# Kernel tuning notes

Measured on AMD Instinct MI355X. Metric: run time of the kernel, lower is better.

Reference implementation:

```python
import jax, jax.numpy as jnp
import numpy as np

VOCAB = 100000; D = 300; F_NUM = 768
M = 64; N = 16
SURF_L = 4; CTX_L = 50; DOC_L = 100; BODY_L = 200
HEADS = 5


def _conv_relu_avg(x, W, b):
    # x: [B, L, D] tokens-embedded; conv1d (valid) + relu + global avgpool -> [B, F]
    y = jax.lax.conv_general_dilated(x.transpose(0, 2, 1), W, (1,), 'VALID',
                                     dimension_numbers=('NCH', 'OIH', 'NCH'))
    return jax.nn.relu(y + b[None, :, None]).mean(axis=2)


def _mha(q, k, v, num_heads=HEADS):
    # split-head scaled dot-product attention (no learned projections), q:[Lq,D] k,v:[Lk,D]
    Lq, Dm = q.shape
    hd = Dm // num_heads
    qh = q.reshape(Lq, num_heads, hd).transpose(1, 0, 2)
    kh = k.reshape(k.shape[0], num_heads, hd).transpose(1, 0, 2)
    vh = v.reshape(v.shape[0], num_heads, hd).transpose(1, 0, 2)
    att = jax.nn.softmax(jnp.einsum('hqd,hkd->hqk', qh, kh) * (1.0 / np.sqrt(hd)), axis=-1)
    out = jnp.einsum('hqk,hkd->hqd', att, vh)
    return out.transpose(1, 0, 2).reshape(Lq, Dm)


def _cos(a, b, eps=1e-6):
    na = jnp.maximum(jnp.sqrt((a * a).sum(-1)), eps)
    nb = jnp.maximum(jnp.sqrt((b * b).sum(-1)), eps)
    return (a * b).sum(-1) / (na * nb)


def setup_inputs() -> dict:
    key = jax.random.key(0)
    ks = jax.random.split(key, 20)
    inp = {}
    inp['mention_entity'] = jnp.ones((M, N), dtype=jnp.int32)
    inp['m'] = M
    inp['n'] = N
    inp['mention_vec'] = jax.random.randint(ks[0], (M, SURF_L), 0, VOCAB)
    inp['context_vec'] = jax.random.randint(ks[1], (M, CTX_L), 0, VOCAB)
    inp['doc_vec'] = jax.random.randint(ks[2], (DOC_L,), 0, VOCAB)
    inp['title_vec'] = jax.random.normal(ks[3], (N, F_NUM), dtype=jnp.float32)
    inp['body_vec'] = jax.random.randint(ks[4], (N, BODY_L), 0, VOCAB)
    inp['sfeats'] = jnp.zeros((N, 1), dtype=jnp.float32)
    inp['m2c_prior'] = jax.random.uniform(ks[5], (N,), dtype=jnp.float32)
    inp['men2cands'] = jax.random.randint(ks[6], (M, N), 0, VOCAB)
    inp['contexts_ids'] = jax.random.randint(ks[7], (M, CTX_L), 0, VOCAB)
    inp['hand_features'] = jax.random.uniform(ks[8], (N, 1), dtype=jnp.float32)
    inp['bert_doc_vec'] = jax.random.normal(ks[9], (1, F_NUM), dtype=jnp.float32)
    # learned parameters
    inp['embed_table'] = jax.random.normal(ks[10], (VOCAB, D), dtype=jnp.float32) * 0.1
    inp['conv_ms_w'] = jax.random.normal(ks[11], (F_NUM, D, 2), dtype=jnp.float32) * 0.05
    inp['conv_ms_b'] = jnp.zeros((F_NUM,), dtype=jnp.float32)
    inp['conv_mc_w'] = jax.random.normal(ks[12], (F_NUM, D, 5), dtype=jnp.float32) * 0.05
    inp['conv_mc_b'] = jnp.zeros((F_NUM,), dtype=jnp.float32)
    inp['layer_local_w'] = jax.random.normal(ks[13], (7,), dtype=jnp.float32) * 0.3
    inp['layer_local_b'] = jnp.zeros((), dtype=jnp.float32)
    inp['att_w1'] = jax.random.normal(ks[14], (600, 300), dtype=jnp.float32) * 0.05
    inp['att_b1'] = jnp.zeros((300,), dtype=jnp.float32)
    inp['att_w2'] = jax.random.normal(ks[15], (300, 1), dtype=jnp.float32) * 0.05
    inp['att_b2'] = jnp.zeros((), dtype=jnp.float32)
    return inp


def reference(mention_entity, m, n, mention_vec, context_vec, doc_vec, title_vec,
              body_vec, sfeats, m2c_prior, men2cands, contexts_ids, hand_features,
              bert_doc_vec, embed_table, conv_ms_w, conv_ms_b, conv_mc_w, conv_mc_b,
              layer_local_w, layer_local_b, att_w1, att_b1, att_w2, att_b2):
    # per-mention conv features (vectorized over all mentions at once)
    ms = _conv_relu_avg(embed_table[mention_vec], conv_ms_w, conv_ms_b)   # [M,768]
    mc = _conv_relu_avg(embed_table[context_vec], conv_mc_w, conv_mc_b)   # [M,768]
    md = bert_doc_vec[0]                                                  # [768]
    doc_emb = embed_table[doc_vec]                                        # [100,300]
    body_emb = embed_table[body_vec]                                      # [N,200,300]

    # per-candidate cross attention doc<->body, max-pooled over query positions
    att_d_b = jax.vmap(lambda b: _mha(doc_emb, b, b).max(axis=0))(body_emb)          # [N,300]
    att_b_d = jax.vmap(lambda b: _mha(b, doc_emb, doc_emb).max(axis=0))(body_emb)    # [N,300]
    comb = jnp.concatenate([att_d_b, att_b_d], axis=-1)                              # [N,600]
    att_score = jax.nn.sigmoid(jax.nn.relu(comb @ att_w1 + att_b1) @ att_w2 + att_b2)[:, 0]  # [N]

    # LocalCtxAttRanker: candidate-vs-context attention score
    ctx_emb = embed_table[contexts_ids]                                   # [M,50,300]
    cand_emb = embed_table[men2cands]                                     # [M,N,300]
    tok = jnp.einsum('mnd,mtd->mnt', cand_emb, ctx_emb)                   # [M,N,50]
    p = jax.nn.softmax(tok.max(axis=1), axis=-1)                          # [M,50]
    ctxv = jnp.einsum('mt,mtd->md', p, ctx_emb)                           # [M,300]
    local_att = jnp.einsum('mnd,md->mn', cand_emb, ctxv)                  # [M,N]

    cos_st = _cos(ms[:, None, :], title_vec[None, :, :])                  # [M,N]
    cos_dt = _cos(md[None, :], title_vec)                                 # [N]
    cos_ct = _cos(mc[:, None, :], title_vec[None, :, :])                  # [M,N]

    Mm = ms.shape[0]
    bc = lambda v: jnp.broadcast_to(v[None, :], (Mm, v.shape[0]))
    # feature order matches torch.cat((hand_fea, prior, localAtt, attScore, C_score))
    feats = jnp.stack([bc(hand_features[:, 0]), bc(m2c_prior), local_att,
                       bc(att_score), cos_st, bc(cos_dt), cos_ct], axis=-1)  # [M,N,7]
    score = feats @ layer_local_w + layer_local_b                         # [M,N]

    # per-mention standardization (unbiased std, as torch.std), softmax and uniform renorm
    mu = score.mean(axis=1, keepdims=True)
    sd = score.std(axis=1, keepdims=True, ddof=1)
    z = (score - mu) / sd
    sm = jax.nn.softmax(z, axis=1)
    zmin = z.min(axis=1, keepdims=True)
    zmax = z.max(axis=1, keepdims=True)
    u = (z + 1.0 - zmin) / (zmax - zmin)
    u = u / u.sum(axis=1, keepdims=True)
    return (z, sm, u)
```

## Files before the change

### kernel.cpp

```cpp
#include <hip/hip_runtime.h>

#define MM 64
#define NN 16
#define DDIM 300
#define FNUM 768
#define SURF_LL 4
#define CTX_LL 50
#define DOC_LL 100
#define BODY_LL 200
#define NHEADS 5
#define HDIM 60

#define GM 2944
#define GK 1536
#define GN 768

typedef unsigned short u16;
typedef unsigned int u32;
typedef __attribute__((ext_vector_type(8))) short short8;
typedef __attribute__((ext_vector_type(4))) float f32x4;

#define OFF_MSG    0
#define OFF_CTX2G  76800
#define OFF_CANDG  1036800
#define OFF_MS     1344000
#define OFF_MC     1393152
#define OFF_PV0    1442304
#define OFF_PV1    1461504
#define OFF_ASC    1495104
#define OFF_LATT   1495120
#define OFF_ABF    1496144
#define OFF_WTMC   (OFF_ABF + GM*GK/2)
#define OFF_WTMS   (OFF_WTMC + GN*GK/2)

__device__ __forceinline__ u16 f2bf(float x) {
  union { float f; u32 u; } v; v.f = x;
  u32 r = v.u + 0x7FFFu + ((v.u >> 16) & 1u);
  return (u16)(r >> 16);
}

#define PREP_GATHER_END  1313
#define PREP_MCZ_END     1361
#define PREP_LOGIT       1361
#define PREP_ABUILD_BEG  1362
#define PREP_ABUILD_END  3570
#define PREP_WTMC_END    4338
#define PREP_WTMS_END    4458

__global__ __launch_bounds__(256) void mega_prep_kernel(
    const float* __restrict__ embed,
    const int* __restrict__ mention_vec,
    const int* __restrict__ context_vec,
    const int* __restrict__ contexts_ids,
    const int* __restrict__ men2cands,
    const float* __restrict__ Wmc,
    const float* __restrict__ Wms,
    float* __restrict__ dst, float* __restrict__ mc,
    float* __restrict__ att_logit,
    u32* __restrict__ Abf, u32* __restrict__ WTmc, float* __restrict__ WTms) {
  __shared__ float psm[4160];
  int bid = blockIdx.x;
  int tid = threadIdx.x;
  if (bid < PREP_GATHER_END) {
    int e4 = bid * 256 + tid;
    if (e4 < 4480 * 75) {
      int row = e4 / 75, c4 = e4 - row * 75;
      int tok;
      if (row < 256)       tok = mention_vec[row];
      else if (row < 3456) tok = contexts_ids[row - 256];
      else                 tok = men2cands[row - 3456];
      float4 v = *(const float4*)(embed + (size_t)tok * DDIM + c4 * 4);
      *(float4*)(dst + (size_t)row * DDIM + c4 * 4) = v;
    }
  } else if (bid < PREP_MCZ_END) {
    int e4 = (bid - PREP_GATHER_END) * 256 + tid;
    *(float4*)(mc + e4 * 4) = make_float4(0.f, 0.f, 0.f, 0.f);
  } else if (bid == PREP_LOGIT) {
    if (tid < NN) att_logit[tid] = 0.f;
  } else if (bid < PREP_ABUILD_END) {
    int idx4 = (bid - PREP_ABUILD_BEG) * 256 + tid;
    int r = idx4 / (GK / 8);
    int kq = idx4 - r * (GK / 8);
    int m = r / 46, t = r - m * 46;
    int kbase = kq * 8;
    u32 wlo[4];
#pragma unroll
    for (int q = 0; q < 4; q++) {
      u32 outw = 0;
#pragma unroll
      for (int j = 0; j < 2; j++) {
        int kj = kbase + q * 2 + j;
        u16 h = 0;
        if (kj < 1500) {
          int tap = kj / 300;
          int d = kj - tap * 300;
          int tok = context_vec[m * CTX_LL + t + tap];
          h = f2bf(embed[(size_t)tok * DDIM + d]);
        }
        outw |= (u32)h << (16 * j);
      }
      wlo[q] = outw;
    }
    ((uint4*)Abf)[idx4] = make_uint4(wlo[0], wlo[1], wlo[2], wlo[3]);
  } else if (bid < PREP_WTMC_END) {
    int n = bid - PREP_ABUILD_END;
    for (int i = tid; i < 1500; i += 256) psm[i] = Wmc[(size_t)n * 1500 + i];
    __syncthreads();
    for (int kp = tid; kp < GK / 2; kp += 256) {
      u32 outw = 0;
#pragma unroll
      for (int j = 0; j < 2; j++) {
        int kj = kp * 2 + j;
        u16 h = 0;
        if (kj < 1500) {
          int tap = kj / 300;
          int d = kj - tap * 300;
          h = f2bf(psm[d * 5 + tap]);
        }
        outw |= (u32)h << (16 * j);
      }
      WTmc[(size_t)n * (GK / 2) + kp] = outw;
    }
  } else {
    int tile = bid - PREP_WTMC_END;
    int kt = tile / 12, ft = tile - kt * 12;
    int k0 = kt * 64, f0 = ft * 64;
    for (int idx = tid; idx < 64 * 64; idx += 256) {
      int i = idx >> 6, j = idx & 63;
      if (k0 + j < 600)
        psm[j * 65 + i] = Wms[(size_t)(f0 + i) * 600 + (k0 + j)];
    }
    __syncthreads();
    for (int idx = tid; idx < 64 * 64; idx += 256) {
      int j = idx >> 6, i = idx & 63;
      if (k0 + j < 600)
        WTms[(size_t)(k0 + j) * FNUM + (f0 + i)] = psm[j * 65 + i];
    }
  }
}

__device__ __forceinline__ void conv_gemm_body(
    const u16* __restrict__ A,
    const u16* __restrict__ B,
    const float* __restrict__ bias,
    float* __restrict__ mc, int g, float* __restrict__ smem) {
  int bn = g % (GN / 64), bm = g / (GN / 64);
  u16* As = (u16*)smem;
  u16* Bs = (u16*)(smem + 2304);
  int tid = threadIdx.x;
  int w = tid >> 6, lane = tid & 63;
  int wr = w >> 1, wc = w & 1;
  int lg = lane >> 4, lm = lane & 15;
  f32x4 acc[2][2];
#pragma unroll
  for (int i = 0; i < 2; i++)
#pragma unroll
    for (int j = 0; j < 2; j++) acc[i][j] = (f32x4)0.f;
  int c0row = tid >> 3, ck = (tid & 7) * 8;
  const u16* Ag = A + (size_t)(bm * 64) * GK;
  const u16* Bg = B + (size_t)(bn * 64) * GK;
  for (int kt = 0; kt < GK / 64; kt++) {
    int k0 = kt * 64;
    uint4 av0 = *(const uint4*)(Ag + (size_t)c0row * GK + k0 + ck);
    uint4 av1 = *(const uint4*)(Ag + (size_t)(c0row + 32) * GK + k0 + ck);
    uint4 bv0 = *(const uint4*)(Bg + (size_t)c0row * GK + k0 + ck);
    uint4 bv1 = *(const uint4*)(Bg + (size_t)(c0row + 32) * GK + k0 + ck);
    __syncthreads();
    *(uint4*)&As[c0row * 72 + ck] = av0;
    *(uint4*)&As[(c0row + 32) * 72 + ck] = av1;
    *(uint4*)&Bs[c0row * 72 + ck] = bv0;
    *(uint4*)&Bs[(c0row + 32) * 72 + ck] = bv1;
    __syncthreads();
#pragma unroll
    for (int kk = 0; kk < 2; kk++) {
      short8 af0 = *(const short8*)&As[(wr * 32 + lm) * 72 + kk * 32 + lg * 8];
      short8 af1 = *(const short8*)&As[(wr * 32 + 16 + lm) * 72 + kk * 32 + lg * 8];
      short8 bf0 = *(const short8*)&Bs[(wc * 32 + lm) * 72 + kk * 32 + lg * 8];
      short8 bf1 = *(const short8*)&Bs[(wc * 32 + 16 + lm) * 72 + kk * 32 + lg * 8];
      acc[0][0] = __builtin_amdgcn_mfma_f32_16x16x32_bf16(af0, bf0, acc[0][0], 0, 0, 0);
      acc[0][1] = __builtin_amdgcn_mfma_f32_16x16x32_bf16(af0, bf1, acc[0][1], 0, 0, 0);
      acc[1][0] = __builtin_amdgcn_mfma_f32_16x16x32_bf16(af1, bf0, acc[1][0], 0, 0, 0);
      acc[1][1] = __builtin_amdgcn_mfma_f32_16x16x32_bf16(af1, bf1, acc[1][1], 0, 0, 0);
    }
  }
#pragma unroll
  for (int mf = 0; mf < 2; mf++)
#pragma unroll
    for (int nf = 0; nf < 2; nf++) {
      int col = bn * 64 + wc * 32 + nf * 16 + lm;
      float bb = bias[col];
      int base = bm * 64 + wr * 32 + mf * 16 + lg * 4;
      int mcur = base / 46;
      float s = 0.f;
#pragma unroll
      for (int r = 0; r < 4; r++) {
        float v = fmaxf(acc[mf][nf][r] + bb, 0.f) * (1.0f / 46.0f);
        int mm = (base + r) / 46;
        if (mm != mcur) { atomicAdd(&mc[mcur * FNUM + col], s); s = 0.f; mcur = mm; }
        s += v;
      }
      atomicAdd(&mc[mcur * FNUM + col], s);
    }
}

__device__ __forceinline__ void conv_ms_body(
    const float* __restrict__ msg, const float* __restrict__ WT,
    const float* __restrict__ B, float* __restrict__ ms, int b) {
  int m = b / 3, fi = b - m * 3;
  int f = fi * 256 + threadIdx.x;
  const float* x = msg + m * SURF_LL * DDIM;
  float a0 = 0.f, a1 = 0.f, a2 = 0.f;
  for (int d = 0; d < DDIM; d++) {
    float v0 = x[d], v1 = x[DDIM + d], v2 = x[2 * DDIM + d], v3 = x[3 * DDIM + d];
    float wA = WT[(size_t)(2 * d) * FNUM + f];
    float wB = WT[(size_t)(2 * d + 1) * FNUM + f];
    a0 += v0 * wA + v1 * wB;
    a1 += v1 * wA + v2 * wB;
    a2 += v2 * wA + v3 * wB;
  }
  float bb = B[f];
  float r = fmaxf(a0 + bb, 0.f) + fmaxf(a1 + bb, 0.f) + fmaxf(a2 + bb, 0.f);
  ms[m * FNUM + f] = r * (1.0f / 3.0f);
}

template <int DIR>
__device__ __forceinline__ void scores_pv_body(
    const float* __restrict__ embed, const int* __restrict__ doc_vec,
    const int* __restrict__ body_vec, float* __restrict__ pvp, int b,
    float* __restrict__ smem) {
  constexpr int Lq = DIR ? 200 : 100;
  constexpr int Lk = DIR ? 100 : 200;
  constexpr int KPL = DIR ? 2 : 4;
  constexpr int NQT = DIR ? 7 : 4;
  constexpr int NHALF = DIR ? 1 : 2;
  int qt = b / 80;
  int rem = b - qt * 80;
  int n = rem / 5, h = rem - n * 5;
  const int* qids = DIR ? body_vec + n * BODY_LL : doc_vec;
  const int* kids = DIR ? doc_vec : body_vec + n * BODY_LL;
  float* Ks = smem;
  float* Qs = smem + 12400;
  float* Pl = smem + 12400;
  float* red = smem + 15600;
  for (int idx = threadIdx.x; idx < Lk * 15; idx += 256) {
    int r = idx / 15, c = idx - r * 15;
    float4 v = *(const float4*)(embed + (size_t)kids[r] * DDIM + h * HDIM + c * 4);
    float* dp = Ks + r * 62 + c * 4;
    dp[0] = v.x; dp[1] = v.y; dp[2] = v.z; dp[3] = v.w;
  }
  for (int idx = threadIdx.x; idx < 32 * 15; idx += 256) {
    int r = idx / 15, c = idx - r * 15;
    int q = qt * 32 + r; if (q >= Lq) q = Lq - 1;
    float4 v = *(const float4*)(embed + (size_t)qids[q] * DDIM + h * HDIM + c * 4);
    float* dp = Qs + r * 64 + c * 4;
    dp[0] = v.x; dp[1] = v.y; dp[2] = v.z; dp[3] = v.w;
  }
  __syncthreads();
  int w = threadIdx.x >> 6, lane = threadIdx.x & 63;
  int kcl[KPL];
#pragma unroll
  for (int j = 0; j < KPL; j++) {
    int kk = lane + 64 * j; kcl[j] = (kk < Lk) ? kk : (Lk - 1);
  }
  float acc[8][KPL];
#pragma unroll
  for (int i = 0; i < 8; i++)
#pragma unroll
    for (int j = 0; j < KPL; j++) acc[i][j] = 0.f;
  for (int d = 0; d < HDIM; d += 4) {
    float2 kva[KPL], kvb[KPL];
#pragma unroll
    for (int j = 0; j < KPL; j++) {
      kva[j] = *(const float2*)&Ks[kcl[j] * 62 + d];
      kvb[j] = *(const float2*)&Ks[kcl[j] * 62 + d + 2];
    }
#pragma unroll
    for (int i = 0; i < 8; i++) {
      float4 qv = *(const float4*)&Qs[(w * 8 + i) * 64 + d];
#pragma unroll
      for (int j = 0; j < KPL; j++)
        acc[i][j] += qv.x * kva[j].x + qv.y * kva[j].y +
                     qv.z * kvb[j].x + qv.w * kvb[j].y;
    }
  }
  const float scale = 0.12909944487358056f;
#pragma unroll
  for (int i = 0; i < 8; i++) {
    float mx = -1e30f;
#pragma unroll
    for (int j = 0; j < KPL; j++)
      if (lane + 64 * j < Lk) mx = fmaxf(mx, acc[i][j]);
#pragma unroll
    for (int o = 32; o >= 1; o >>= 1) mx = fmaxf(mx, __shfl_xor(mx, o));
    float mxs = mx * scale;
    float p[KPL];
    float s = 0.f;
#pragma unroll
    for (int j = 0; j < KPL; j++) {
      p[j] = (lane + 64 * j < Lk) ? __expf(acc[i][j] * scale - mxs) : 0.f;
      s += p[j];
    }
#pragma unroll
    for (int o = 32; o >= 1; o >>= 1) s += __shfl_xor(s, o);
    float inv = 1.0f / s;
#pragma unroll
    for (int j = 0; j < KPL; j++) acc[i][j] = p[j] * inv;
  }
  __syncthreads();
  float o[8];
#pragma unroll
  for (int i = 0; i < 8; i++) o[i] = 0.f;
  int dl = (lane < HDIM) ? lane : (HDIM - 1);
#pragma unroll
  for (int half = 0; half < NHALF; half++) {
    int kbase = half * 100;
#pragma unroll
    for (int j = 0; j < KPL; j++) {
      int kk = lane + 64 * j;
      int rel = kk - kbase;
      if (rel >= 0 && rel < 100 && kk < Lk) {
#pragma unroll
        for (int i = 0; i < 8; i++)
          Pl[(w * 8 + i) * 100 + rel] = acc[i][j];
      }
    }
    for (int k4 = 0; k4 < 25; k4++) {
      int k = kbase + k4 * 4;
      float kv0 = Ks[(k + 0) * 62 + dl];
      float kv1 = Ks[(k + 1) * 62 + dl];
      float kv2 = Ks[(k + 2) * 62 + dl];
      float kv3 = Ks[(k + 3) * 62 + dl];
#pragma unroll
      for (int i = 0; i < 8; i++) {
        float4 pq = *(const float4*)&Pl[(w * 8 + i) * 100 + k4 * 4];
        o[i] += pq.x * kv0 + pq.y * kv1 + pq.z * kv2 + pq.w * kv3;
      }
    }
  }
  float omax = -1e30f;
#pragma unroll
  for (int i = 0; i < 8; i++) {
    int q = qt * 32 + w * 8 + i;
    if (q < Lq) omax = fmaxf(omax, o[i]);
  }
  red[w * 64 + lane] = omax;
  __syncthreads();
  if (threadIdx.x < 64 && lane < HDIM) {
    float m4 = fmaxf(fmaxf(red[0 * 64 + lane], red[1 * 64 + lane]),
                     fmaxf(red[2 * 64 + lane], red[3 * 64 + lane]));
    pvp[((size_t)(n * NHEADS + h) * NQT + qt) * HDIM + lane] = m4;
  }
}

__device__ __forceinline__ void tokctxv_body(
    const float* __restrict__ candg, const float* __restrict__ ctx2g,
    float* __restrict__ local_att, int m, float* __restrict__ smem) {
  float* cand  = smem;
  float* ctx   = smem + 4800;
  float* tokb  = smem + 9600;
  float* tkmx  = smem + 9872;
  float* pp    = smem + 9936;
  float* sctxv = smem + 10000;
  int tid = threadIdx.x;
  for (int i = tid; i < NN * DDIM; i += 256)
    cand[i] = candg[(size_t)m * NN * DDIM + i];
  int nI = tid >> 4, tt = tid & 15;
  for (int tile = 0; tile < 4; tile++) {
    int cbase = tile * 16;
    __syncthreads();
    for (int i = tid; i < 16 * DDIM; i += 256) {
      int rr = i / DDIM, cc = i - rr * DDIM;
      int t = cbase + rr;
      ctx[rr * DDIM + cc] = (t < CTX_LL) ? ctx2g[(size_t)(m * CTX_LL + t) * DDIM + cc] : 0.f;
    }
    __syncthreads();
    const float4* ca = (const float4*)(cand + nI * DDIM);
    const float4* cb = (const float4*)(ctx + tt * DDIM);
    float dsum = 0.f;
#pragma unroll
    for (int c = 0; c < 75; c++) {
      float4 a = ca[c], b = cb[c];
      dsum += a.x * b.x + a.y * b.y + a.z * b.z + a.w * b.w;
    }
    tokb[nI * 17 + tt] = dsum;
    __syncthreads();
    if (tid < 16) {
      float mx = -1e30f;
      for (int nn = 0; nn < NN; nn++) mx = fmaxf(mx, tokb[nn * 17 + tid]);
      int t = cbase + tid;
      if (t < CTX_LL) tkmx[t] = mx;
    }
  }
  __syncthreads();
  if (tid < 64) {
    float v = (tid < CTX_LL) ? tkmx[tid] : -1e30f;
    float mx = v;
#pragma unroll
    for (int o = 32; o >= 1; o >>= 1) mx = fmaxf(mx, __shfl_xor(mx, o));
    float e = (tid < CTX_LL) ? expf(v - mx) : 0.f;
    float s = e;
#pragma unroll
    for (int o = 32; o >= 1; o >>= 1) s += __shfl_xor(s, o);
    pp[tid] = e / s;
  }
  __syncthreads();
  for (int d = tid; d < DDIM; d += 256) {
    float acc = 0.f;
    for (int t = 0; t < CTX_LL; t++)
      acc += pp[t] * ctx2g[(size_t)(m * CTX_LL + t) * DDIM + d];
    sctxv[d] = acc;
  }
  __syncthreads();
  int j = tid & 15;
  float dd = 0.f;
  for (int i = j; i < DDIM; i += 16) dd += cand[nI * DDIM + i] * sctxv[i];
#pragma unroll
  for (int o = 8; o >= 1; o >>= 1) dd += __shfl_xor(dd, o);
  if (j == 0) local_att[m * NN + nI] = dd;
}

__global__ __launch_bounds__(256) void mega_mid_kernel(
    const float* __restrict__ embed,
    const int* __restrict__ doc_vec,
    const int* __restrict__ body_vec,
    const float* __restrict__ msg,
    const float* __restrict__ WTms,
    const float* __restrict__ Bms,
    const float* __restrict__ candg,
    const float* __restrict__ ctx2g,
    const u16* __restrict__ Abf,
    const u16* __restrict__ WTmc,
    const float* __restrict__ Bmc,
    float* __restrict__ ms,
    float* __restrict__ mc,
    float* __restrict__ pv0,
    float* __restrict__ pv1,
    float* __restrict__ local_att) {
  __shared__ float smem[15856];
  int bid = blockIdx.x;
  if (bid < 192) {
    conv_ms_body(msg, WTms, Bms, ms, bid);
  } else if (bid < 512) {
    scores_pv_body<0>(embed, doc_vec, body_vec, pv0, bid - 192, smem);
  } else if (bid < 1072) {
    scores_pv_body<1>(embed, doc_vec, body_vec, pv1, bid - 512, smem);
  } else if (bid < 1136) {
    tokctxv_body(candg, ctx2g, local_att, bid - 1072, smem);
  } else {
    conv_gemm_body(Abf, WTmc, Bmc, mc, bid - 1136, smem);
  }
}

__global__ __launch_bounds__(256) void mlp_kernel(
    const float* __restrict__ pv0, const float* __restrict__ pv1,
    const float* __restrict__ w1, const float* __restrict__ b1,
    const float* __restrict__ w2,
    float* __restrict__ att_logit) {
  int bid = blockIdx.x;
  int n = bid / 5, jc = bid - n * 5;
  int tid = threadIdx.x;
  __shared__ float comb[600];
  __shared__ float partial[4][64];
  for (int idx = tid; idx < 600; idx += 256) {
    int side = idx >= 300;
    int pos = idx - side * 300;
    int h = pos / 60, d = pos - h * 60;
    float mx = -1e30f;
    if (!side) {
#pragma unroll
      for (int pt = 0; pt < 4; pt++)
        mx = fmaxf(mx, pv0[(size_t)((n * NHEADS + h) * 4 + pt) * HDIM + d]);
    } else {
#pragma unroll
      for (int pt = 0; pt < 7; pt++)
        mx = fmaxf(mx, pv1[(size_t)((n * NHEADS + h) * 7 + pt) * HDIM + d]);
    }
    comb[idx] = mx;
  }
  __syncthreads();
  int w = tid >> 6, lane = tid & 63;
  int jl = (lane < 60) ? lane : 59;
  int jg = jc * 60 + jl;
  float acc = 0.f;
  for (int k = w; k < 600; k += 4)
    acc += comb[k] * w1[(size_t)k * 300 + jg];
  partial[w][lane] = acc;
  __syncthreads();
  if (tid < 64) {
    float hv = partial[0][lane] + partial[1][lane] +
               partial[2][lane] + partial[3][lane];
    float hj = fmaxf(hv + b1[jg], 0.f) * w2[jg];
    if (lane >= 60) hj = 0.f;
#pragma unroll
    for (int o = 32; o >= 1; o >>= 1) hj += __shfl_xor(hj, o);
    if (lane == 0) atomicAdd(&att_logit[n], hj);
  }
}

__global__ __launch_bounds__(256) void final_kernel(
    const float* __restrict__ ms,
    const float* __restrict__ mc,
    const float* __restrict__ title,
    const float* __restrict__ bert,
    const float* __restrict__ att_logit,
    const float* __restrict__ b2,
    const float* __restrict__ m2c_prior,
    const float* __restrict__ hand,
    const float* __restrict__ local_att,
    const float* __restrict__ w7,
    const float* __restrict__ b7,
    float* __restrict__ out) {
  int m = blockIdx.x, tid = threadIdx.x;
  __shared__ float sms[FNUM], smc[FNUM], smd[FNUM];
  __shared__ float snorm[3], sscore[16], wred[3][4];
  for (int i = tid; i < FNUM; i += 256) {
    sms[i] = ms[m * FNUM + i];
    smc[i] = mc[m * FNUM + i];
    smd[i] = bert[i];
  }
  __syncthreads();
  float p1 = 0.f, p2 = 0.f, p3 = 0.f;
  for (int i = tid; i < FNUM; i += 256) {
    float a = sms[i], b = smc[i], c = smd[i];
    p1 += a * a; p2 += b * b; p3 += c * c;
  }
#pragma unroll
  for (int o = 32; o >= 1; o >>= 1) {
    p1 += __shfl_xor(p1, o); p2 += __shfl_xor(p2, o); p3 += __shfl_xor(p3, o);
  }
  int wid = tid >> 6, lane = tid & 63;
  if (lane == 0) { wred[0][wid] = p1; wred[1][wid] = p2; wred[2][wid] = p3; }
  __syncthreads();
  if (tid == 0) {
    snorm[0] = fmaxf(sqrtf(wred[0][0] + wred[0][1] + wred[0][2] + wred[0][3]), 1e-6f);
    snorm[1] = fmaxf(sqrtf(wred[1][0] + wred[1][1] + wred[1][2] + wred[1][3]), 1e-6f);
    snorm[2] = fmaxf(sqrtf(wred[2][0] + wred[2][1] + wred[2][2] + wred[2][3]), 1e-6f);
  }
  __syncthreads();
  int nI = tid >> 4, j = tid & 15;
  float d1 = 0.f, d2 = 0.f, d3 = 0.f, d4 = 0.f;
  for (int i = j; i < FNUM; i += 16) {
    float t = title[nI * FNUM + i];
    d1 += sms[i] * t; d2 += smc[i] * t; d3 += smd[i] * t; d4 += t * t;
  }
#pragma unroll
  for (int o = 8; o >= 1; o >>= 1) {
    d1 += __shfl_xor(d1, o); d2 += __shfl_xor(d2, o);
    d3 += __shfl_xor(d3, o); d4 += __shfl_xor(d4, o);
  }
  if (j == 0) {
    float nt = fmaxf(sqrtf(d4), 1e-6f);
    float cos_st = d1 / (snorm[0] * nt);
    float cos_ct = d2 / (snorm[1] * nt);
    float cos_dt = d3 / (snorm[2] * nt);
    float asc = 1.0f / (1.0f + expf(-(att_logit[nI] + b2[0])));
    float score = hand[nI] * w7[0] + m2c_prior[nI] * w7[1] +
                  local_att[m * NN + nI] * w7[2] + asc * w7[3] +
                  cos_st * w7[4] + cos_dt * w7[5] + cos_ct * w7[6] + b7[0];
    sscore[nI] = score;
  }
  __syncthreads();
  if (tid < 16) {
    float x = sscore[tid];
    float s = x;
#pragma unroll
    for (int o = 8; o >= 1; o >>= 1) s += __shfl_xor(s, o);
    float mu = s * (1.0f / 16.0f);
    float dv = (x - mu) * (x - mu);
    float vs = dv;
#pragma unroll
    for (int o = 8; o >= 1; o >>= 1) vs += __shfl_xor(vs, o);
    float sd = sqrtf(vs * (1.0f / 15.0f));
    float z = (x - mu) / sd;
    float zm = z;
#pragma unroll
    for (int o = 8; o >= 1; o >>= 1) zm = fmaxf(zm, __shfl_xor(zm, o));
    float e = expf(z - zm);
    float es = e;
#pragma unroll
    for (int o = 8; o >= 1; o >>= 1) es += __shfl_xor(es, o);
    float sm = e / es;
    float zmin = z;
#pragma unroll
    for (int o = 8; o >= 1; o >>= 1) zmin = fminf(zmin, __shfl_xor(zmin, o));
    float u0 = (z + 1.0f - zmin) / (zm - zmin);
    float us = u0;
#pragma unroll
    for (int o = 8; o >= 1; o >>= 1) us += __shfl_xor(us, o);
    float u = u0 / us;
    out[m * NN + tid] = z;
    out[MM * NN + m * NN + tid] = sm;
    out[2 * MM * NN + m * NN + tid] = u;
  }
}

extern "C" void kernel_launch(void* const* d_in, const int* in_sizes, int n_in,
                              void* d_out, int out_size, void* d_ws, size_t ws_size,
                              hipStream_t stream) {
  const int*   mention_vec   = (const int*)d_in[3];
  const int*   context_vec   = (const int*)d_in[4];
  const int*   doc_vec       = (const int*)d_in[5];
  const float* title_vec     = (const float*)d_in[6];
  const int*   body_vec      = (const int*)d_in[7];
  const float* m2c_prior     = (const float*)d_in[9];
  const int*   men2cands     = (const int*)d_in[10];
  const int*   contexts_ids  = (const int*)d_in[11];
  const float* hand_features = (const float*)d_in[12];
  const float* bert_doc_vec  = (const float*)d_in[13];
  const float* embed_table   = (const float*)d_in[14];
  const float* conv_ms_w     = (const float*)d_in[15];
  const float* conv_ms_b     = (const float*)d_in[16];
  const float* conv_mc_w     = (const float*)d_in[17];
  const float* conv_mc_b     = (const float*)d_in[18];
  const float* layer_local_w = (const float*)d_in[19];
  const float* layer_local_b = (const float*)d_in[20];
  const float* att_w1        = (const float*)d_in[21];
  const float* att_b1        = (const float*)d_in[22];
  const float* att_w2        = (const float*)d_in[23];
  const float* att_b2        = (const float*)d_in[24];

  float* ws     = (float*)d_ws;
  float* msg    = ws + OFF_MSG;
  float* ctx2g  = ws + OFF_CTX2G;
  float* candg  = ws + OFF_CANDG;
  float* ms     = ws + OFF_MS;
  float* mc     = ws + OFF_MC;
  float* pv0    = ws + OFF_PV0;
  float* pv1    = ws + OFF_PV1;
  float* att_lg = ws + OFF_ASC;
  float* latt   = ws + OFF_LATT;
  u16*   Abf    = (u16*)(ws + OFF_ABF);
  u16*   WTmc   = (u16*)(ws + OFF_WTMC);
  float* WTms   = ws + OFF_WTMS;
  float* out    = (float*)d_out;

  mega_prep_kernel<<<dim3(PREP_WTMS_END), dim3(256), 0, stream>>>(
      embed_table, mention_vec, context_vec, contexts_ids, men2cands,
      conv_mc_w, conv_ms_w, ws, mc, att_lg, (u32*)Abf, (u32*)WTmc, WTms);
  mega_mid_kernel<<<dim3(1688), dim3(256), 0, stream>>>(
      embed_table, doc_vec, body_vec, msg, WTms, conv_ms_b, candg, ctx2g,
      Abf, WTmc, conv_mc_b, ms, mc, pv0, pv1, latt);
  mlp_kernel<<<dim3(80), dim3(256), 0, stream>>>(
      pv0, pv1, att_w1, att_b1, att_w2, att_lg);
  final_kernel<<<dim3(MM), dim3(256), 0, stream>>>(
      ms, mc, title_vec, bert_doc_vec, att_lg, att_b2, m2c_prior,
      hand_features, latt, layer_local_w, layer_local_b, out);
}
```

Measured before the change: 376.3 us.

## Launch mid kernel with 512 threads and split attention rows across eight waves

Doubles the mid mega-kernel block size to 512 threads. The attention score/PV body now spreads its 32 query rows over eight waves of four rows each instead of four waves of eight, and reduces the per-wave maxima across eight waves. The GEMM body uses the extra threads only for tile loads, and the conv_ms and tokctxv bodies mostly mask off or duplicate work in the upper half. This is meant to cut per-wave serial work and register pressure in the attention path, at the cost of idle or redundant waves in the other bodies and a tighter register budget under the 512-thread launch bound.

Result: slower. 439.4 us (+16.7%).

```diff
diff --git a/kernel.cpp b/kernel.cpp
--- a/kernel.cpp
+++ b/kernel.cpp
@@ -149,7 +149,7 @@
   u16* Bs = (u16*)(smem + 2304);
   int tid = threadIdx.x;
   int w = tid >> 6, lane = tid & 63;
-  int wr = w >> 1, wc = w & 1;
+  int wr = (w >> 1) & 1, wc = w & 1;
   int lg = lane >> 4, lm = lane & 15;
   f32x4 acc[2][2];
 #pragma unroll
@@ -161,53 +161,53 @@
   const u16* Bg = B + (size_t)(bn * 64) * GK;
   for (int kt = 0; kt < GK / 64; kt++) {
     int k0 = kt * 64;
-    uint4 av0 = *(const uint4*)(Ag + (size_t)c0row * GK + k0 + ck);
-    uint4 av1 = *(const uint4*)(Ag + (size_t)(c0row + 32) * GK + k0 + ck);
-    uint4 bv0 = *(const uint4*)(Bg + (size_t)c0row * GK + k0 + ck);
-    uint4 bv1 = *(const uint4*)(Bg + (size_t)(c0row + 32) * GK + k0 + ck);
+    uint4 av = *(const uint4*)(Ag + (size_t)c0row * GK + k0 + ck);
+    uint4 bv = *(const uint4*)(Bg + (size_t)c0row * GK + k0 + ck);
     __syncthreads();
-    *(uint4*)&As[c0row * 72 + ck] = av0;
-    *(uint4*)&As[(c0row + 32) * 72 + ck] = av1;
-    *(uint4*)&Bs[c0row * 72 + ck] = bv0;
-    *(uint4*)&Bs[(c0row + 32) * 72 + ck] = bv1;
+    *(uint4*)&As[c0row * 72 + ck] = av;
+    *(uint4*)&Bs[c0row * 72 + ck] = bv;
     __syncthreads();
-#pragma unroll
-    for (int kk = 0; kk < 2; kk++) {
-      short8 af0 = *(const short8*)&As[(wr * 32 + lm) * 72 + kk * 32 + lg * 8];
-      short8 af1 = *(const short8*)&As[(wr * 32 + 16 + lm) * 72 + kk * 32 + lg * 8];
-      short8 bf0 = *(const short8*)&Bs[(wc * 32 + lm) * 72 + kk * 32 + lg * 8];
-      short8 bf1 = *(const short8*)&Bs[(wc * 32 + 16 + lm) * 72 + kk * 32 + lg * 8];
-      acc[0][0] = __builtin_amdgcn_mfma_f32_16x16x32_bf16(af0, bf0, acc[0][0], 0, 0, 0);
-      acc[0][1] = __builtin_amdgcn_mfma_f32_16x16x32_bf16(af0, bf1, acc[0][1], 0, 0, 0);
-      acc[1][0] = __builtin_amdgcn_mfma_f32_16x16x32_bf16(af1, bf0, acc[1][0], 0, 0, 0);
-      acc[1][1] = __builtin_amdgcn_mfma_f32_16x16x32_bf16(af1, bf1, acc[1][1], 0, 0, 0);
-    }
-  }
-#pragma unroll
-  for (int mf = 0; mf < 2; mf++)
-#pragma unroll
-    for (int nf = 0; nf < 2; nf++) {
-      int col = bn * 64 + wc * 32 + nf * 16 + lm;
-      float bb = bias[col];
-      int base = bm * 64 + wr * 32 + mf * 16 + lg * 4;
-      int mcur = base / 46;
-      float s = 0.f;
-#pragma unroll
-      for (int r = 0; r < 4; r++) {
-        float v = fmaxf(acc[mf][nf][r] + bb, 0.f) * (1.0f / 46.0f);
-        int mm = (base + r) / 46;
-        if (mm != mcur) { atomicAdd(&mc[mcur * FNUM + col], s); s = 0.f; mcur = mm; }
-        s += v;
+    if (w < 4) {
+#pragma unroll
+      for (int kk = 0; kk < 2; kk++) {
+        short8 af0 = *(const short8*)&As[(wr * 32 + lm) * 72 + kk * 32 + lg * 8];
+        short8 af1 = *(const short8*)&As[(wr * 32 + 16 + lm) * 72 + kk * 32 + lg * 8];
+        short8 bf0 = *(const short8*)&Bs[(wc * 32 + lm) * 72 + kk * 32 + lg * 8];
+        short8 bf1 = *(const short8*)&Bs[(wc * 32 + 16 + lm) * 72 + kk * 32 + lg * 8];
+        acc[0][0] = __builtin_amdgcn_mfma_f32_16x16x32_bf16(af0, bf0, acc[0][0], 0, 0, 0);
+        acc[0][1] = __builtin_amdgcn_mfma_f32_16x16x32_bf16(af0, bf1, acc[0][1], 0, 0, 0);
+        acc[1][0] = __builtin_amdgcn_mfma_f32_16x16x32_bf16(af1, bf0, acc[1][0], 0, 0, 0);
+        acc[1][1] = __builtin_amdgcn_mfma_f32_16x16x32_bf16(af1, bf1, acc[1][1], 0, 0, 0);
       }
-      atomicAdd(&mc[mcur * FNUM + col], s);
-    }
+    }
+  }
+  if (w < 4) {
+#pragma unroll
+    for (int mf = 0; mf < 2; mf++)
+#pragma unroll
+      for (int nf = 0; nf < 2; nf++) {
+        int col = bn * 64 + wc * 32 + nf * 16 + lm;
+        float bb = bias[col];
+        int base = bm * 64 + wr * 32 + mf * 16 + lg * 4;
+        int mcur = base / 46;
+        float s = 0.f;
+#pragma unroll
+        for (int r = 0; r < 4; r++) {
+          float v = fmaxf(acc[mf][nf][r] + bb, 0.f) * (1.0f / 46.0f);
+          int mm = (base + r) / 46;
+          if (mm != mcur) { atomicAdd(&mc[mcur * FNUM + col], s); s = 0.f; mcur = mm; }
+          s += v;
+        }
+        atomicAdd(&mc[mcur * FNUM + col], s);
+      }
+  }
 }
 
 __device__ __forceinline__ void conv_ms_body(
     const float* __restrict__ msg, const float* __restrict__ WT,
     const float* __restrict__ B, float* __restrict__ ms, int b) {
   int m = b / 3, fi = b - m * 3;
-  int f = fi * 256 + threadIdx.x;
+  int f = fi * 256 + (threadIdx.x & 255);
   const float* x = msg + m * SURF_LL * DDIM;
   float a0 = 0.f, a1 = 0.f, a2 = 0.f;
   for (int d = 0; d < DDIM; d++) {
@@ -220,7 +220,7 @@
   }
   float bb = B[f];
   float r = fmaxf(a0 + bb, 0.f) + fmaxf(a1 + bb, 0.f) + fmaxf(a2 + bb, 0.f);
-  ms[m * FNUM + f] = r * (1.0f / 3.0f);
+  if (threadIdx.x < 256) ms[m * FNUM + f] = r * (1.0f / 3.0f);
 }
 
 template <int DIR>
@@ -242,13 +242,13 @@
   float* Qs = smem + 12400;
   float* Pl = smem + 12400;
   float* red = smem + 15600;
-  for (int idx = threadIdx.x; idx < Lk * 15; idx += 256) {
+  for (int idx = threadIdx.x; idx < Lk * 15; idx += 512) {
     int r = idx / 15, c = idx - r * 15;
     float4 v = *(const float4*)(embed + (size_t)kids[r] * DDIM + h * HDIM + c * 4);
     float* dp = Ks + r * 62 + c * 4;
     dp[0] = v.x; dp[1] = v.y; dp[2] = v.z; dp[3] = v.w;
   }
-  for (int idx = threadIdx.x; idx < 32 * 15; idx += 256) {
+  for (int idx = threadIdx.x; idx < 32 * 15; idx += 512) {
     int r = idx / 15, c = idx - r * 15;
     int q = qt * 32 + r; if (q >= Lq) q = Lq - 1;
     float4 v = *(const float4*)(embed + (size_t)qids[q] * DDIM + h * HDIM + c * 4);
@@ -262,9 +262,9 @@
   for (int j = 0; j < KPL; j++) {
     int kk = lane + 64 * j; kcl[j] = (kk < Lk) ? kk : (Lk - 1);
   }
-  float acc[8][KPL];
-#pragma unroll
-  for (int i = 0; i < 8; i++)
+  float acc[4][KPL];
+#pragma unroll
+  for (int i = 0; i < 4; i++)
 #pragma unroll
     for (int j = 0; j < KPL; j++) acc[i][j] = 0.f;
   for (int d = 0; d < HDIM; d += 4) {
@@ -275,8 +275,8 @@
       kvb[j] = *(const float2*)&Ks[kcl[j] * 62 + d + 2];
     }
 #pragma unroll
-    for (int i = 0; i < 8; i++) {
-      float4 qv = *(const float4*)&Qs[(w * 8 + i) * 64 + d];
+    for (int i = 0; i < 4; i++) {
+      float4 qv = *(const float4*)&Qs[(w * 4 + i) * 64 + d];
 #pragma unroll
       for (int j = 0; j < KPL; j++)
         acc[i][j] += qv.x * kva[j].x + qv.y * kva[j].y +
@@ -285,7 +285,7 @@
   }
   const float scale = 0.12909944487358056f;
 #pragma unroll
-  for (int i = 0; i < 8; i++) {
+  for (int i = 0; i < 4; i++) {
     float mx = -1e30f;
 #pragma unroll
     for (int j = 0; j < KPL; j++)
@@ -307,9 +307,9 @@
     for (int j = 0; j < KPL; j++) acc[i][j] = p[j] * inv;
   }
   __syncthreads();
-  float o[8];
-#pragma unroll
-  for (int i = 0; i < 8; i++) o[i] = 0.f;
+  float o[4];
+#pragma unroll
+  for (int i = 0; i < 4; i++) o[i] = 0.f;
   int dl = (lane < HDIM) ? lane : (HDIM - 1);
 #pragma unroll
   for (int half = 0; half < NHALF; half++) {
@@ -320,8 +320,8 @@
       int rel = kk - kbase;
       if (rel >= 0 && rel < 100 && kk < Lk) {
 #pragma unroll
-        for (int i = 0; i < 8; i++)
-          Pl[(w * 8 + i) * 100 + rel] = acc[i][j];
+        for (int i = 0; i < 4; i++)
+          Pl[(w * 4 + i) * 100 + rel] = acc[i][j];
       }
     }
     for (int k4 = 0; k4 < 25; k4++) {
@@ -331,23 +331,24 @@
       float kv2 = Ks[(k + 2) * 62 + dl];
       float kv3 = Ks[(k + 3) * 62 + dl];
 #pragma unroll
-      for (int i = 0; i < 8; i++) {
-        float4 pq = *(const float4*)&Pl[(w * 8 + i) * 100 + k4 * 4];
+      for (int i = 0; i < 4; i++) {
+        float4 pq = *(const float4*)&Pl[(w * 4 + i) * 100 + k4 * 4];
         o[i] += pq.x * kv0 + pq.y * kv1 + pq.z * kv2 + pq.w * kv3;
       }
     }
   }
   float omax = -1e30f;
 #pragma unroll
-  for (int i = 0; i < 8; i++) {
-    int q = qt * 32 + w * 8 + i;
+  for (int i = 0; i < 4; i++) {
+    int q = qt * 32 + w * 4 + i;
     if (q < Lq) omax = fmaxf(omax, o[i]);
   }
   red[w * 64 + lane] = omax;
   __syncthreads();
   if (threadIdx.x < 64 && lane < HDIM) {
-    float m4 = fmaxf(fmaxf(red[0 * 64 + lane], red[1 * 64 + lane]),
-                     fmaxf(red[2 * 64 + lane], red[3 * 64 + lane]));
+    float m4 = red[lane];
+#pragma unroll
+    for (int ww = 1; ww < 8; ww++) m4 = fmaxf(m4, red[ww * 64 + lane]);
     pvp[((size_t)(n * NHEADS + h) * NQT + qt) * HDIM + lane] = m4;
   }
 }
@@ -362,13 +363,14 @@
   float* pp    = smem + 9936;
   float* sctxv = smem + 10000;
   int tid = threadIdx.x;
-  for (int i = tid; i < NN * DDIM; i += 256)
+  int t2 = tid & 255;
+  for (int i = tid; i < NN * DDIM; i += 512)
     cand[i] = candg[(size_t)m * NN * DDIM + i];
-  int nI = tid >> 4, tt = tid & 15;
+  int nI = t2 >> 4, tt = t2 & 15;
   for (int tile = 0; tile < 4; tile++) {
     int cbase = tile * 16;
     __syncthreads();
-    for (int i = tid; i < 16 * DDIM; i += 256) {
+    for (int i = tid; i < 16 * DDIM; i += 512) {
       int rr = i / DDIM, cc = i - rr * DDIM;
       int t = cbase + rr;
       ctx[rr * DDIM + cc] = (t < CTX_LL) ? ctx2g[(size_t)(m * CTX_LL + t) * DDIM + cc] : 0.f;
@@ -404,22 +406,22 @@
     pp[tid] = e / s;
   }
   __syncthreads();
-  for (int d = tid; d < DDIM; d += 256) {
+  for (int d = tid; d < DDIM; d += 512) {
     float acc = 0.f;
     for (int t = 0; t < CTX_LL; t++)
       acc += pp[t] * ctx2g[(size_t)(m * CTX_LL + t) * DDIM + d];
     sctxv[d] = acc;
   }
   __syncthreads();
-  int j = tid & 15;
+  int j = t2 & 15;
   float dd = 0.f;
   for (int i = j; i < DDIM; i += 16) dd += cand[nI * DDIM + i] * sctxv[i];
 #pragma unroll
   for (int o = 8; o >= 1; o >>= 1) dd += __shfl_xor(dd, o);
-  if (j == 0) local_att[m * NN + nI] = dd;
-}
-
-__global__ __launch_bounds__(256) void mega_mid_kernel(
+  if (j == 0 && tid < 256) local_att[m * NN + nI] = dd;
+}
+
+__global__ __launch_bounds__(512) void mega_mid_kernel(
     const float* __restrict__ embed,
     const int* __restrict__ doc_vec,
     const int* __restrict__ body_vec,
@@ -436,7 +438,7 @@
     float* __restrict__ pv0,
     float* __restrict__ pv1,
     float* __restrict__ local_att) {
-  __shared__ float smem[15856];
+  __shared__ float smem[16112];
   int bid = blockIdx.x;
   if (bid < 192) {
     conv_ms_body(msg, WTms, Bms, ms, bid);
@@ -637,7 +639,7 @@
   mega_prep_kernel<<<dim3(PREP_WTMS_END), dim3(256), 0, stream>>>(
       embed_table, mention_vec, context_vec, contexts_ids, men2cands,
       conv_mc_w, conv_ms_w, ws, mc, att_lg, (u32*)Abf, (u32*)WTmc, WTms);
-  mega_mid_kernel<<<dim3(1688), dim3(256), 0, stream>>>(
+  mega_mid_kernel<<<dim3(1688), dim3(512), 0, stream>>>(
       embed_table, doc_vec, body_vec, msg, WTms, conv_ms_b, candg, ctx2g,
       Abf, WTmc, conv_mc_b, ms, mc, pv0, pv1, latt);
   mlp_kernel<<<dim3(80), dim3(256), 0, stream>>>(
```

## Split doc-query attention over key halves and shrink mid-kernel shared memory

Applied to the files above, without the earlier changes.

The doc-to-body attention (200 keys) is now split into two 100-key blocks, each storing unnormalized partial outputs plus softmax max and sum. The MLP kernel merges these flash-style before taking the per-position max. The candidate tile in the local-attention body is read straight from global memory instead of being staged in LDS. Together these cut the mid kernel's static shared memory from about 62KB to 38KB, raising occupancy and adding parallel blocks. The cost is extra partial-result traffic and a serial 100-step merge loop per element in the MLP kernel.

Measured after the change: 469.9 us. +24.9%, slower.

```diff
diff --git a/kernel.cpp b/kernel.cpp
--- a/kernel.cpp
+++ b/kernel.cpp
@@ -25,13 +25,14 @@
 #define OFF_CANDG  1036800
 #define OFF_MS     1344000
 #define OFF_MC     1393152
-#define OFF_PV0    1442304
 #define OFF_PV1    1461504
 #define OFF_ASC    1495104
 #define OFF_LATT   1495120
 #define OFF_ABF    1496144
 #define OFF_WTMC   (OFF_ABF + GM*GK/2)
 #define OFF_WTMS   (OFF_WTMC + GN*GK/2)
+#define OFF_PV0P   4807760
+#define PV0P_UNIT  1984
 
 __device__ __forceinline__ u16 f2bf(float x) {
   union { float f; u32 u; } v; v.f = x;
@@ -223,26 +224,19 @@
   ms[m * FNUM + f] = r * (1.0f / 3.0f);
 }
 
-template <int DIR>
-__device__ __forceinline__ void scores_pv_body(
+template <int MODE>
+__device__ __forceinline__ void attn_body(
     const float* __restrict__ embed, const int* __restrict__ doc_vec,
-    const int* __restrict__ body_vec, float* __restrict__ pvp, int b,
-    float* __restrict__ smem) {
-  constexpr int Lq = DIR ? 200 : 100;
-  constexpr int Lk = DIR ? 100 : 200;
-  constexpr int KPL = DIR ? 2 : 4;
-  constexpr int NQT = DIR ? 7 : 4;
-  constexpr int NHALF = DIR ? 1 : 2;
-  int qt = b / 80;
-  int rem = b - qt * 80;
-  int n = rem / 5, h = rem - n * 5;
-  const int* qids = DIR ? body_vec + n * BODY_LL : doc_vec;
-  const int* kids = DIR ? doc_vec : body_vec + n * BODY_LL;
+    const int* __restrict__ body_vec, float* __restrict__ outp,
+    int qt, int n, int h, int khalf, float* __restrict__ smem) {
+  constexpr int Lq = MODE ? 200 : 100;
+  const int* qids = MODE ? body_vec + n * BODY_LL : doc_vec;
+  const int* kids = MODE ? doc_vec : body_vec + n * BODY_LL + khalf * 100;
   float* Ks = smem;
-  float* Qs = smem + 12400;
-  float* Pl = smem + 12400;
-  float* red = smem + 15600;
-  for (int idx = threadIdx.x; idx < Lk * 15; idx += 256) {
+  float* Qs = smem + 6200;
+  float* Pl = smem + 6200;
+  float* red = smem + 9400;
+  for (int idx = threadIdx.x; idx < 100 * 15; idx += 256) {
     int r = idx / 15, c = idx - r * 15;
     float4 v = *(const float4*)(embed + (size_t)kids[r] * DDIM + h * HDIM + c * 4);
     float* dp = Ks + r * 62 + c * 4;
@@ -257,54 +251,42 @@
   }
   __syncthreads();
   int w = threadIdx.x >> 6, lane = threadIdx.x & 63;
-  int kcl[KPL];
-#pragma unroll
-  for (int j = 0; j < KPL; j++) {
-    int kk = lane + 64 * j; kcl[j] = (kk < Lk) ? kk : (Lk - 1);
-  }
-  float acc[8][KPL];
-#pragma unroll
-  for (int i = 0; i < 8; i++)
-#pragma unroll
-    for (int j = 0; j < KPL; j++) acc[i][j] = 0.f;
+  int kc0 = lane;
+  bool k1ok = (lane + 64 < 100);
+  int kc1 = k1ok ? lane + 64 : 99;
+  float acc[8][2];
+#pragma unroll
+  for (int i = 0; i < 8; i++) { acc[i][0] = 0.f; acc[i][1] = 0.f; }
   for (int d = 0; d < HDIM; d += 4) {
-    float2 kva[KPL], kvb[KPL];
-#pragma unroll
-    for (int j = 0; j < KPL; j++) {
-      kva[j] = *(const float2*)&Ks[kcl[j] * 62 + d];
-      kvb[j] = *(const float2*)&Ks[kcl[j] * 62 + d + 2];
-    }
+    float2 a0 = *(const float2*)&Ks[kc0 * 62 + d];
+    float2 b0 = *(const float2*)&Ks[kc0 * 62 + d + 2];
+    float2 a1 = *(const float2*)&Ks[kc1 * 62 + d];
+    float2 b1 = *(const float2*)&Ks[kc1 * 62 + d + 2];
 #pragma unroll
     for (int i = 0; i < 8; i++) {
       float4 qv = *(const float4*)&Qs[(w * 8 + i) * 64 + d];
-#pragma unroll
-      for (int j = 0; j < KPL; j++)
-        acc[i][j] += qv.x * kva[j].x + qv.y * kva[j].y +
-                     qv.z * kvb[j].x + qv.w * kvb[j].y;
+      acc[i][0] += qv.x * a0.x + qv.y * a0.y + qv.z * b0.x + qv.w * b0.y;
+      acc[i][1] += qv.x * a1.x + qv.y * a1.y + qv.z * b1.x + qv.w * b1.y;
     }
   }
   const float scale = 0.12909944487358056f;
+  float msv[8], ssv[8];
 #pragma unroll
   for (int i = 0; i < 8; i++) {
-    float mx = -1e30f;
-#pragma unroll
-    for (int j = 0; j < KPL; j++)
-      if (lane + 64 * j < Lk) mx = fmaxf(mx, acc[i][j]);
+    float mx = acc[i][0];
+    if (k1ok) mx = fmaxf(mx, acc[i][1]);
 #pragma unroll
     for (int o = 32; o >= 1; o >>= 1) mx = fmaxf(mx, __shfl_xor(mx, o));
     float mxs = mx * scale;
-    float p[KPL];
-    float s = 0.f;
-#pragma unroll
-    for (int j = 0; j < KPL; j++) {
-      p[j] = (lane + 64 * j < Lk) ? __expf(acc[i][j] * scale - mxs) : 0.f;
-      s += p[j];
-    }
+    float p0 = __expf(acc[i][0] * scale - mxs);
+    float p1 = k1ok ? __expf(acc[i][1] * scale - mxs) : 0.f;
+    float s = p0 + p1;
 #pragma unroll
     for (int o = 32; o >= 1; o >>= 1) s += __shfl_xor(s, o);
+    msv[i] = mxs; ssv[i] = s;
     float inv = 1.0f / s;
-#pragma unroll
-    for (int j = 0; j < KPL; j++) acc[i][j] = p[j] * inv;
+    acc[i][0] = p0 * inv;
+    acc[i][1] = p1 * inv;
   }
   __syncthreads();
   float o[8];
@@ -312,59 +294,64 @@
   for (int i = 0; i < 8; i++) o[i] = 0.f;
   int dl = (lane < HDIM) ? lane : (HDIM - 1);
 #pragma unroll
-  for (int half = 0; half < NHALF; half++) {
-    int kbase = half * 100;
-#pragma unroll
-    for (int j = 0; j < KPL; j++) {
-      int kk = lane + 64 * j;
-      int rel = kk - kbase;
-      if (rel >= 0 && rel < 100 && kk < Lk) {
-#pragma unroll
-        for (int i = 0; i < 8; i++)
-          Pl[(w * 8 + i) * 100 + rel] = acc[i][j];
+  for (int i = 0; i < 8; i++) Pl[(w * 8 + i) * 100 + lane] = acc[i][0];
+  if (k1ok) {
+#pragma unroll
+    for (int i = 0; i < 8; i++) Pl[(w * 8 + i) * 100 + lane + 64] = acc[i][1];
+  }
+  for (int k4 = 0; k4 < 25; k4++) {
+    int k = k4 * 4;
+    float kv0 = Ks[(k + 0) * 62 + dl];
+    float kv1 = Ks[(k + 1) * 62 + dl];
+    float kv2 = Ks[(k + 2) * 62 + dl];
+    float kv3 = Ks[(k + 3) * 62 + dl];
+#pragma unroll
+    for (int i = 0; i < 8; i++) {
+      float4 pq = *(const float4*)&Pl[(w * 8 + i) * 100 + k4 * 4];
+      o[i] += pq.x * kv0 + pq.y * kv1 + pq.z * kv2 + pq.w * kv3;
+    }
+  }
+  if constexpr (MODE == 0) {
+    if (lane < HDIM) {
+#pragma unroll
+      for (int i = 0; i < 8; i++)
+        outp[(w * 8 + i) * HDIM + lane] = o[i];
+    }
+    if (lane == 0) {
+#pragma unroll
+      for (int i = 0; i < 8; i++) {
+        outp[1920 + w * 8 + i] = msv[i];
+        outp[1952 + w * 8 + i] = ssv[i];
       }
     }
-    for (int k4 = 0; k4 < 25; k4++) {
-      int k = kbase + k4 * 4;
-      float kv0 = Ks[(k + 0) * 62 + dl];
-      float kv1 = Ks[(k + 1) * 62 + dl];
-      float kv2 = Ks[(k + 2) * 62 + dl];
-      float kv3 = Ks[(k + 3) * 62 + dl];
-#pragma unroll
-      for (int i = 0; i < 8; i++) {
-        float4 pq = *(const float4*)&Pl[(w * 8 + i) * 100 + k4 * 4];
-        o[i] += pq.x * kv0 + pq.y * kv1 + pq.z * kv2 + pq.w * kv3;
-      }
-    }
-  }
-  float omax = -1e30f;
-#pragma unroll
-  for (int i = 0; i < 8; i++) {
-    int q = qt * 32 + w * 8 + i;
-    if (q < Lq) omax = fmaxf(omax, o[i]);
-  }
-  red[w * 64 + lane] = omax;
-  __syncthreads();
-  if (threadIdx.x < 64 && lane < HDIM) {
-    float m4 = fmaxf(fmaxf(red[0 * 64 + lane], red[1 * 64 + lane]),
-                     fmaxf(red[2 * 64 + lane], red[3 * 64 + lane]));
-    pvp[((size_t)(n * NHEADS + h) * NQT + qt) * HDIM + lane] = m4;
+  } else {
+    float omax = -1e30f;
+#pragma unroll
+    for (int i = 0; i < 8; i++) {
+      int q = qt * 32 + w * 8 + i;
+      if (q < Lq) omax = fmaxf(omax, o[i]);
+    }
+    red[w * 64 + lane] = omax;
+    __syncthreads();
+    if (threadIdx.x < 64 && lane < HDIM) {
+      float m4 = fmaxf(fmaxf(red[0 * 64 + lane], red[1 * 64 + lane]),
+                       fmaxf(red[2 * 64 + lane], red[3 * 64 + lane]));
+      outp[((size_t)(n * NHEADS + h) * 7 + qt) * HDIM + lane] = m4;
+    }
   }
 }
 
 __device__ __forceinline__ void tokctxv_body(
     const float* __restrict__ candg, const float* __restrict__ ctx2g,
     float* __restrict__ local_att, int m, float* __restrict__ smem) {
-  float* cand  = smem;
-  float* ctx   = smem + 4800;
-  float* tokb  = smem + 9600;
-  float* tkmx  = smem + 9872;
-  float* pp    = smem + 9936;
-  float* sctxv = smem + 10000;
+  float* ctx   = smem;
+  float* tokb  = smem + 4800;
+  float* tkmx  = smem + 5072;
+  float* pp    = smem + 5136;
+  float* sctxv = smem + 5200;
   int tid = threadIdx.x;
-  for (int i = tid; i < NN * DDIM; i += 256)
-    cand[i] = candg[(size_t)m * NN * DDIM + i];
   int nI = tid >> 4, tt = tid & 15;
+  const float* cand = candg + (size_t)m * NN * DDIM;
   for (int tile = 0; tile < 4; tile++) {
     int cbase = tile * 16;
     __syncthreads();
@@ -433,26 +420,37 @@
     const float* __restrict__ Bmc,
     float* __restrict__ ms,
     float* __restrict__ mc,
-    float* __restrict__ pv0,
+    float* __restrict__ pv0p,
     float* __restrict__ pv1,
     float* __restrict__ local_att) {
-  __shared__ float smem[15856];
+  __shared__ float smem[9656];
   int bid = blockIdx.x;
   if (bid < 192) {
     conv_ms_body(msg, WTms, Bms, ms, bid);
-  } else if (bid < 512) {
-    scores_pv_body<0>(embed, doc_vec, body_vec, pv0, bid - 192, smem);
-  } else if (bid < 1072) {
-    scores_pv_body<1>(embed, doc_vec, body_vec, pv1, bid - 512, smem);
-  } else if (bid < 1136) {
-    tokctxv_body(candg, ctx2g, local_att, bid - 1072, smem);
+  } else if (bid < 832) {
+    int s = bid - 192;
+    int qt = s / 160;
+    int r = s - qt * 160;
+    int n = r / 10;
+    int rr = r - n * 10;
+    int h = rr >> 1, half = rr & 1;
+    float* up = pv0p + (size_t)(((qt * 16 + n) * NHEADS + h) * 2 + half) * PV0P_UNIT;
+    attn_body<0>(embed, doc_vec, body_vec, up, qt, n, h, half, smem);
+  } else if (bid < 1392) {
+    int b = bid - 832;
+    int qt = b / 80;
+    int rem = b - qt * 80;
+    int n = rem / 5, h = rem - n * 5;
+    attn_body<1>(embed, doc_vec, body_vec, pv1, qt, n, h, 0, smem);
+  } else if (bid < 1456) {
+    tokctxv_body(candg, ctx2g, local_att, bid - 1392, smem);
   } else {
-    conv_gemm_body(Abf, WTmc, Bmc, mc, bid - 1136, smem);
+    conv_gemm_body(Abf, WTmc, Bmc, mc, bid - 1456, smem);
   }
 }
 
 __global__ __launch_bounds__(256) void mlp_kernel(
-    const float* __restrict__ pv0, const float* __restrict__ pv1,
+    const float* __restrict__ pv0p, const float* __restrict__ pv1,
     const float* __restrict__ w1, const float* __restrict__ b1,
     const float* __restrict__ w2,
     float* __restrict__ att_logit) {
@@ -467,9 +465,18 @@
     int h = pos / 60, d = pos - h * 60;
     float mx = -1e30f;
     if (!side) {
-#pragma unroll
-      for (int pt = 0; pt < 4; pt++)
-        mx = fmaxf(mx, pv0[(size_t)((n * NHEADS + h) * 4 + pt) * HDIM + d]);
+      for (int q = 0; q < DOC_LL; q++) {
+        int qt = q >> 5, i = q & 31;
+        const float* u1 = pv0p + (size_t)(((qt * 16 + n) * NHEADS + h) * 2 + 0) * PV0P_UNIT;
+        const float* u2 = u1 + PV0P_UNIT;
+        float m1 = u1[1920 + i], s1 = u1[1952 + i];
+        float m2 = u2[1920 + i], s2 = u2[1952 + i];
+        float M = fmaxf(m1, m2);
+        float wa = s1 * __expf(m1 - M);
+        float wb = s2 * __expf(m2 - M);
+        float o = (wa * u1[i * HDIM + d] + wb * u2[i * HDIM + d]) / (wa + wb);
+        mx = fmaxf(mx, o);
+      }
     } else {
 #pragma unroll
       for (int pt = 0; pt < 7; pt++)
@@ -625,23 +632,23 @@
   float* candg  = ws + OFF_CANDG;
   float* ms     = ws + OFF_MS;
   float* mc     = ws + OFF_MC;
-  float* pv0    = ws + OFF_PV0;
   float* pv1    = ws + OFF_PV1;
   float* att_lg = ws + OFF_ASC;
   float* latt   = ws + OFF_LATT;
   u16*   Abf    = (u16*)(ws + OFF_ABF);
   u16*   WTmc   = (u16*)(ws + OFF_WTMC);
   float* WTms   = ws + OFF_WTMS;
+  float* pv0p   = ws + OFF_PV0P;
   float* out    = (float*)d_out;
 
   mega_prep_kernel<<<dim3(PREP_WTMS_END), dim3(256), 0, stream>>>(
       embed_table, mention_vec, context_vec, contexts_ids, men2cands,
       conv_mc_w, conv_ms_w, ws, mc, att_lg, (u32*)Abf, (u32*)WTmc, WTms);
-  mega_mid_kernel<<<dim3(1688), dim3(256), 0, stream>>>(
+  mega_mid_kernel<<<dim3(2008), dim3(256), 0, stream>>>(
       embed_table, doc_vec, body_vec, msg, WTms, conv_ms_b, candg, ctx2g,
-      Abf, WTmc, conv_mc_b, ms, mc, pv0, pv1, latt);
+      Abf, WTmc, conv_mc_b, ms, mc, pv0p, pv1, latt);
   mlp_kernel<<<dim3(80), dim3(256), 0, stream>>>(
-      pv0, pv1, att_w1, att_b1, att_w2, att_lg);
+      pv0p, pv1, att_w1, att_b1, att_w2, att_lg);
   final_kernel<<<dim3(MM), dim3(256), 0, stream>>>(
       ms, mc, title_vec, bert_doc_vec, att_lg, att_b2, m2c_prior,
       hand_features, latt, layer_local_w, layer_local_b, out);
```
